# Performance work log

Hardware: AMD Instinct MI355X
Metric: run time of the kernel (lower is better)

## Reference

```python
import jax, jax.numpy as jnp
import numpy as np

# Planck radiance in wavenumber form: B(nu, T) = c1*nu^3 / (exp(c2*nu/T) - 1)
# nu in cm^-1, T in Kelvin, B in W / (m^2 sr cm^-1)
C1 = 1.191042e-8
C2 = 1.4387752
N_TEMPS = 20


def planck_radiance(nu, T):
    return C1 * nu ** 3 / jnp.expm1(C2 * nu / T)


def setup_inputs() -> dict:
    key = jax.random.key(0)
    k1, k2, k3 = jax.random.split(key, 3)
    N, C = 1048576, 54  # 1024x1024 pixels, 54 spectral channels
    wg = jnp.linspace(720.0, 1250.0, C, dtype=jnp.float32)
    v = (wg - wg.min()) / (wg.max() - wg.min())
    pi = 3.14159
    library = jnp.stack([
        jnp.full((C,), 0.98),                      # skin
        0.9 + 0.05 * jnp.sin(2 * pi * v),          # fabric_cotton
        0.15 + 0.1 * v,                            # metal_aluminum
        0.95 - 0.03 * v,                           # vegetation
        0.92 + 0.02 * jnp.sin(4 * pi * v),         # concrete
        0.85 + 0.1 * v,                            # glass
    ]).astype(jnp.float32)
    # realistic LWIR radiance magnitudes (~0.02-0.12 W/m^2/sr/cm^-1)
    s_sky = 0.05 * jax.random.uniform(k1, (C,), dtype=jnp.float32)
    s_ground = 0.08 + 0.02 * jax.random.uniform(k2, (C,), dtype=jnp.float32)
    s_obs = 0.02 + 0.1 * jax.random.uniform(k3, (N, C), dtype=jnp.float32)
    return {"s_obs": s_obs, "s_sky": s_sky, "s_ground": s_ground,
            "library": library, "wavenumber_grid": wg}


def reference(s_obs, s_sky, s_ground, library, wavenumber_grid):
    N, C = s_obs.shape
    M = library.shape[0]
    t_cand = jnp.linspace(250.0, 350.0, N_TEMPS, dtype=s_obs.dtype)
    # All candidate model spectra are pixel-independent (V fixed at 0.5):
    x_amb = 0.5 * s_sky + 0.5 * s_ground                           # [C]
    B = planck_radiance(wavenumber_grid[None, :], t_cand[:, None])  # [T, C]
    s_model = library[:, None, :] * B[None, :, :] \
        + (1.0 - library[:, None, :]) * x_amb                       # [M, T, C]
    cand = s_model.reshape(M * N_TEMPS, C)  # row-major: idx = m*T + t, matches loop order
    # ||s_obs - cand||^2 expanded: memory-bound [N, M*T] loss matrix
    losses = (jnp.sum(s_obs ** 2, axis=-1, keepdims=True)
              - 2.0 * s_obs @ cand.T
              + jnp.sum(cand ** 2, axis=-1))                        # [N, M*T]
    best = jnp.argmin(losses, axis=-1)                              # first-min, matches strict '<'
    best_loss = jnp.take_along_axis(losses, best[:, None], axis=1)[:, 0]
    m_idx = best // N_TEMPS
    t_idx = best % N_TEMPS
    best_t = t_cand[t_idx]                                          # [N]
    best_e = library[m_idx]                                         # [N, C]
    best_v = jnp.full((N,), 0.5, dtype=s_obs.dtype)
    s_recon = best_e * planck_radiance(wavenumber_grid[None, :], best_t[:, None]) \
        + (1.0 - best_e) * x_amb                                    # [N, C]
    texture = best_e.mean(axis=-1)
    beta = jnp.zeros((N, 1), dtype=s_obs.dtype)
    objective = best_loss.mean()
    return (best_t, best_e, best_v, beta, texture, s_recon, objective)
```

## Files before the change

kernel.cpp:

```cpp
#include <hip/hip_runtime.h>
#include <math.h>

#define C_CH 54
#define CP   64
#define NT   20
#define NM   6
#define NK   120
#define BLK  256

typedef float sf16 __attribute__((ext_vector_type(16)));
typedef float sf8  __attribute__((ext_vector_type(8)));

__global__ __launch_bounds__(256) void hadar_prep(
    const float* __restrict__ s_sky, const float* __restrict__ s_ground,
    const float* __restrict__ library, const float* __restrict__ wg,
    float* __restrict__ cand)
{
    __shared__ float xamb[C_CH];
    __shared__ float tc[NT];
    __shared__ float lm[NM];
    const int tid = threadIdx.x;
    if (tid < NT) tc[tid] = 250.0f + (float)tid * (100.0f / 19.0f);
    if (tid < C_CH) xamb[tid] = 0.5f * s_sky[tid] + 0.5f * s_ground[tid];
    if (tid < NM) {
        float s = 0.0f;
        for (int c = 0; c < C_CH; ++c) s += library[tid * C_CH + c];
        lm[tid] = s / (float)C_CH;
    }
    __syncthreads();

    const float c1 = 1.191042e-8f, c2 = 1.4387752f;
    for (int idx = tid; idx < NK * CP; idx += 256) {
        const int k = idx >> 6, c = idx & 63;
        float v = 0.0f;
        if (c < C_CH) {
            const int m = k / NT, t = k - m * NT;
            const float nu = wg[c];
            const float B = c1 * nu * nu * nu / expm1f(c2 * nu / tc[t]);
            const float e = library[m * C_CH + c];
            v = e * B + (1.0f - e) * xamb[c];
        }
        cand[idx] = v;
    }
    __syncthreads();

    if (tid < NK) {
        float s = 0.0f;
        for (int c = 0; c < C_CH; ++c) { float v = cand[tid * CP + c]; s += v * v; }
        const int m = tid / NT, t = tid - m * NT;
        cand[tid * CP + 54] = s;
        cand[tid * CP + 55] = tc[t];
        cand[tid * CP + 56] = lm[m];
    }
}

#define CE(c) ((c) < 16 ? q0[(c)] : (c) < 32 ? q1[(c)-16] : (c) < 48 ? q2[(c)-32] : q3[(c)-48])

__global__ __launch_bounds__(BLK) void hadar_main(
    const float* __restrict__ s_obs,
    const float* __restrict__ library,
    const float* __restrict__ cand,
    float* __restrict__ out, float* __restrict__ partials, int N)
{
    const int tid = threadIdx.x;
    const long long n0 = (long long)blockIdx.x * BLK + tid;
    const bool v0 = (n0 < N);

    float row0[C_CH];
    if (v0) {
        const float2* rp = (const float2*)(s_obs + n0 * C_CH);
        #pragma unroll
        for (int i = 0; i < C_CH / 2; ++i) {
            float2 w = rp[i];
            row0[2 * i] = w.x; row0[2 * i + 1] = w.y;
        }
    } else {
        #pragma unroll
        for (int c = 0; c < C_CH; ++c) row0[c] = 0.0f;
    }

    float ssq0 = 0.0f;
    #pragma unroll
    for (int c = 0; c < C_CH; ++c) ssq0 += row0[c] * row0[c];

    float bl0 = 3.4e38f;
    int bk0 = 0;

    const float* pk = cand;
    #pragma unroll 1
    for (int k = 0; k < NK; ++k, pk += CP) {
        sf16 q0, q1, q2;
        sf8  q3;
        asm volatile("s_load_dwordx16 %0, %1, 0x0"  : "=s"(q0) : "s"(pk));
        asm volatile("s_load_dwordx16 %0, %1, 0x40" : "=s"(q1) : "s"(pk));
        asm volatile("s_load_dwordx16 %0, %1, 0x80" : "=s"(q2) : "s"(pk));
        asm volatile("s_load_dwordx8  %0, %1, 0xc0" : "=s"(q3) : "s"(pk));
        asm volatile("s_waitcnt lgkmcnt(0)" : "+s"(q0), "+s"(q1), "+s"(q2), "+s"(q3));

        float a0[4] = {0.f, 0.f, 0.f, 0.f};
        #pragma unroll
        for (int c = 0; c < C_CH; ++c) {
            a0[c & 3] += row0[c] * CE(c);
        }
        const float sq = q3[6];
        const float d0 = (a0[0] + a0[1]) + (a0[2] + a0[3]);
        const float l0 = (ssq0 - 2.0f * d0) + sq;
        if (l0 < bl0) { bl0 = l0; bk0 = k; }
    }

    const size_t NN = (size_t)N;
    const size_t NC = (size_t)C_CH * NN;
    float lsum = 0.0f;

    if (v0) {
        lsum = bl0;
        const int m = bk0 / NT;
        const float* crow = cand + (size_t)bk0 * CP;

        out[n0] = crow[55];
        out[NN + NC + n0] = 0.5f;
        out[2 * NN + NC + n0] = 0.0f;
        out[3 * NN + NC + n0] = crow[56];

        float2* bep = (float2*)(out + NN + (size_t)n0 * C_CH);
        const float2* lp = (const float2*)(library + m * C_CH);
        #pragma unroll
        for (int i = 0; i < C_CH / 2; ++i) bep[i] = lp[i];

        float2* srp = (float2*)(out + 4 * NN + NC + (size_t)n0 * C_CH);
        const float2* cp2 = (const float2*)crow;
        #pragma unroll
        for (int i = 0; i < C_CH / 2; ++i) srp[i] = cp2[i];
    }

    __shared__ float red[BLK];
    red[tid] = lsum;
    __syncthreads();
    #pragma unroll
    for (int s = BLK / 2; s > 0; s >>= 1) {
        if (tid < s) red[tid] += red[tid + s];
        __syncthreads();
    }
    if (tid == 0) partials[blockIdx.x] = red[0];
}

__global__ __launch_bounds__(256) void hadar_reduce(
    const float* __restrict__ partials, int nb, float* __restrict__ obj_out, float invN)
{
    __shared__ float red[256];
    float s = 0.0f;
    for (int i = threadIdx.x; i < nb; i += 256) s += partials[i];
    red[threadIdx.x] = s;
    __syncthreads();
    #pragma unroll
    for (int st = 128; st > 0; st >>= 1) {
        if (threadIdx.x < st) red[threadIdx.x] += red[threadIdx.x + st];
        __syncthreads();
    }
    if (threadIdx.x == 0) *obj_out = red[0] * invN;
}

extern "C" void kernel_launch(void* const* d_in, const int* in_sizes, int n_in,
                              void* d_out, int out_size, void* d_ws, size_t ws_size,
                              hipStream_t stream)
{
    const float* s_obs    = (const float*)d_in[0];
    const float* s_sky    = (const float*)d_in[1];
    const float* s_ground = (const float*)d_in[2];
    const float* library  = (const float*)d_in[3];
    const float* wg       = (const float*)d_in[4];
    float* out = (float*)d_out;

    const int N  = in_sizes[0] / C_CH;
    const int nb = (N + BLK - 1) / BLK;

    float* ws       = (float*)d_ws;
    float* cand     = ws;
    float* partials = ws + 8192;

    hadar_prep<<<1, 256, 0, stream>>>(s_sky, s_ground, library, wg, cand);
    hadar_main<<<nb, BLK, 0, stream>>>(s_obs, library, cand, out, partials, N);

    const size_t NN = (size_t)N;
    float* obj_out = out + 4 * NN + 2 * (size_t)C_CH * NN;
    hadar_reduce<<<1, 256, 0, stream>>>(partials, nb, obj_out, 1.0f / (float)N);
}
```

Before: 852.1 us.

## Split each pixel across four lanes with DPP reductions and prescaled candidates

The main kernel now gives each pixel's 54-channel dot product to four lanes, each handling 16 channels. Partial sums are combined with DPP quad shuffles, and each lane processes two pixels so every candidate load is reused. Candidates are stored premultiplied by -2, with their squared norm folded in through a constant-1 input lane, which removes the per-candidate scale and add. Candidate data is read with vector loads instead of scalar loads, and writes are spread across lanes for better coalescing. The cost is 128 pixels per block instead of 256, a different rounding order, and redundant candidate loads across lanes.

Result: slower. 1.529 ms (+79.4%).

```diff
diff --git a/kernel.cpp b/kernel.cpp
--- a/kernel.cpp
+++ b/kernel.cpp
@@ -7,9 +7,17 @@
 #define NM   6
 #define NK   120
 #define BLK  256
-
-typedef float sf16 __attribute__((ext_vector_type(16)));
-typedef float sf8  __attribute__((ext_vector_type(8)));
+#define PIXW 32
+#define PPB  128
+
+__device__ __forceinline__ float qxor1(float v) {
+    return __int_as_float(__builtin_amdgcn_update_dpp(
+        __float_as_int(v), __float_as_int(v), 0xB1, 0xF, 0xF, true));
+}
+__device__ __forceinline__ float qxor2(float v) {
+    return __int_as_float(__builtin_amdgcn_update_dpp(
+        __float_as_int(v), __float_as_int(v), 0x4E, 0xF, 0xF, true));
+}
 
 __global__ __launch_bounds__(256) void hadar_prep(
     const float* __restrict__ s_sky, const float* __restrict__ s_ground,
@@ -32,29 +40,25 @@
     const float c1 = 1.191042e-8f, c2 = 1.4387752f;
     for (int idx = tid; idx < NK * CP; idx += 256) {
         const int k = idx >> 6, c = idx & 63;
+        const int m = k / NT, t = k - m * NT;
         float v = 0.0f;
         if (c < C_CH) {
-            const int m = k / NT, t = k - m * NT;
             const float nu = wg[c];
             const float B = c1 * nu * nu * nu / expm1f(c2 * nu / tc[t]);
             const float e = library[m * C_CH + c];
-            v = e * B + (1.0f - e) * xamb[c];
-        }
+            v = -2.0f * (e * B + (1.0f - e) * xamb[c]);
+        } else if (c == 56) v = tc[t];
+        else if (c == 57) v = lm[m];
         cand[idx] = v;
     }
     __syncthreads();
 
     if (tid < NK) {
         float s = 0.0f;
-        for (int c = 0; c < C_CH; ++c) { float v = cand[tid * CP + c]; s += v * v; }
-        const int m = tid / NT, t = tid - m * NT;
-        cand[tid * CP + 54] = s;
-        cand[tid * CP + 55] = tc[t];
-        cand[tid * CP + 56] = lm[m];
-    }
-}
-
-#define CE(c) ((c) < 16 ? q0[(c)] : (c) < 32 ? q1[(c)-16] : (c) < 48 ? q2[(c)-32] : q3[(c)-48])
+        for (int c = 0; c < C_CH; ++c) { float w = cand[tid * CP + c]; s += w * w; }
+        cand[tid * CP + 54] = 0.25f * s;
+    }
+}
 
 __global__ __launch_bounds__(BLK) void hadar_main(
     const float* __restrict__ s_obs,
@@ -62,75 +66,112 @@
     const float* __restrict__ cand,
     float* __restrict__ out, float* __restrict__ partials, int N)
 {
-    const int tid = threadIdx.x;
-    const long long n0 = (long long)blockIdx.x * BLK + tid;
-    const bool v0 = (n0 < N);
-
-    float row0[C_CH];
-    if (v0) {
-        const float2* rp = (const float2*)(s_obs + n0 * C_CH);
-        #pragma unroll
-        for (int i = 0; i < C_CH / 2; ++i) {
-            float2 w = rp[i];
-            row0[2 * i] = w.x; row0[2 * i + 1] = w.y;
-        }
-    } else {
-        #pragma unroll
-        for (int c = 0; c < C_CH; ++c) row0[c] = 0.0f;
-    }
-
-    float ssq0 = 0.0f;
-    #pragma unroll
-    for (int c = 0; c < C_CH; ++c) ssq0 += row0[c] * row0[c];
-
-    float bl0 = 3.4e38f;
-    int bk0 = 0;
-
-    const float* pk = cand;
-    #pragma unroll 1
-    for (int k = 0; k < NK; ++k, pk += CP) {
-        sf16 q0, q1, q2;
-        sf8  q3;
-        asm volatile("s_load_dwordx16 %0, %1, 0x0"  : "=s"(q0) : "s"(pk));
-        asm volatile("s_load_dwordx16 %0, %1, 0x40" : "=s"(q1) : "s"(pk));
-        asm volatile("s_load_dwordx16 %0, %1, 0x80" : "=s"(q2) : "s"(pk));
-        asm volatile("s_load_dwordx8  %0, %1, 0xc0" : "=s"(q3) : "s"(pk));
-        asm volatile("s_waitcnt lgkmcnt(0)" : "+s"(q0), "+s"(q1), "+s"(q2), "+s"(q3));
-
+    const int tid  = threadIdx.x;
+    const int wave = tid >> 6;
+    const int lane = tid & 63;
+    const int px   = lane >> 2;
+    const int g    = lane & 3;
+    const long long nb = (long long)blockIdx.x * PPB + wave * PIXW + px;
+
+    float r[2][16];
+    float ssq[2];
+    #pragma unroll
+    for (int p = 0; p < 2; ++p) {
+        const long long n = nb + p * 16;
+        #pragma unroll
+        for (int j = 0; j < 16; ++j) r[p][j] = 0.0f;
+        if (n < N) {
+            const float* src = s_obs + n * C_CH + g * 16;
+            if (g < 3) {
+                #pragma unroll
+                for (int j = 0; j < 8; ++j) {
+                    float2 w = *(const float2*)(src + 2 * j);
+                    r[p][2 * j] = w.x; r[p][2 * j + 1] = w.y;
+                }
+            } else {
+                #pragma unroll
+                for (int j = 0; j < 3; ++j) {
+                    float2 w = *(const float2*)(src + 2 * j);
+                    r[p][2 * j] = w.x; r[p][2 * j + 1] = w.y;
+                }
+            }
+        }
+        float s = 0.0f;
+        #pragma unroll
+        for (int j = 0; j < 16; ++j) s = fmaf(r[p][j], r[p][j], s);
+        s += qxor1(s);
+        s += qxor2(s);
+        ssq[p] = s;
+        if (g == 3) r[p][6] = 1.0f;
+    }
+
+    float bl[2] = { 3.4e38f, 3.4e38f };
+    int   bk[2] = { 0, 0 };
+
+    const float* cbase = cand + g * 16;
+    #pragma unroll 2
+    for (int k = 0; k < NK; ++k) {
+        const float* cp = cbase + (size_t)k * CP;
+        float cc[16];
+        #pragma unroll
+        for (int j = 0; j < 4; ++j) {
+            float4 w = *(const float4*)(cp + 4 * j);
+            cc[4 * j] = w.x; cc[4 * j + 1] = w.y; cc[4 * j + 2] = w.z; cc[4 * j + 3] = w.w;
+        }
         float a0[4] = {0.f, 0.f, 0.f, 0.f};
-        #pragma unroll
-        for (int c = 0; c < C_CH; ++c) {
-            a0[c & 3] += row0[c] * CE(c);
-        }
-        const float sq = q3[6];
-        const float d0 = (a0[0] + a0[1]) + (a0[2] + a0[3]);
-        const float l0 = (ssq0 - 2.0f * d0) + sq;
-        if (l0 < bl0) { bl0 = l0; bk0 = k; }
+        float a1[4] = {0.f, 0.f, 0.f, 0.f};
+        #pragma unroll
+        for (int j = 0; j < 16; ++j) {
+            a0[j & 3] = fmaf(r[0][j], cc[j], a0[j & 3]);
+            a1[j & 3] = fmaf(r[1][j], cc[j], a1[j & 3]);
+        }
+        float d0 = (a0[0] + a0[1]) + (a0[2] + a0[3]);
+        float d1 = (a1[0] + a1[1]) + (a1[2] + a1[3]);
+        d0 += qxor1(d0); d0 += qxor2(d0);
+        d1 += qxor1(d1); d1 += qxor2(d1);
+        if (d0 < bl[0]) { bl[0] = d0; bk[0] = k; }
+        if (d1 < bl[1]) { bl[1] = d1; bk[1] = k; }
     }
 
     const size_t NN = (size_t)N;
     const size_t NC = (size_t)C_CH * NN;
     float lsum = 0.0f;
-
-    if (v0) {
-        lsum = bl0;
-        const int m = bk0 / NT;
-        const float* crow = cand + (size_t)bk0 * CP;
-
-        out[n0] = crow[55];
-        out[NN + NC + n0] = 0.5f;
-        out[2 * NN + NC + n0] = 0.0f;
-        out[3 * NN + NC + n0] = crow[56];
-
-        float2* bep = (float2*)(out + NN + (size_t)n0 * C_CH);
-        const float2* lp = (const float2*)(library + m * C_CH);
-        #pragma unroll
-        for (int i = 0; i < C_CH / 2; ++i) bep[i] = lp[i];
-
-        float2* srp = (float2*)(out + 4 * NN + NC + (size_t)n0 * C_CH);
-        const float2* cp2 = (const float2*)crow;
-        #pragma unroll
-        for (int i = 0; i < C_CH / 2; ++i) srp[i] = cp2[i];
+    #pragma unroll
+    for (int p = 0; p < 2; ++p) {
+        const long long n = nb + p * 16;
+        if (n >= N) continue;
+        const int k = bk[p];
+        const int m = k / NT;
+        const float* crow = cand + (size_t)k * CP;
+
+        if (g == 0) {
+            out[n]                 = crow[56];
+            out[NN + NC + n]       = 0.5f;
+            out[2 * NN + NC + n]   = 0.0f;
+            out[3 * NN + NC + n]   = crow[57];
+            lsum += ssq[p] + bl[p];
+        }
+
+        const float* lrow = library + m * C_CH;
+        float* eout = out + NN + (size_t)n * C_CH;
+        float* rout = out + 4 * NN + NC + (size_t)n * C_CH;
+        if (g < 3) {
+            #pragma unroll
+            for (int j = 0; j < 8; ++j) {
+                const int c = g * 16 + 2 * j;
+                *(float2*)(eout + c) = *(const float2*)(lrow + c);
+                float2 w = *(const float2*)(crow + c);
+                *(float2*)(rout + c) = make_float2(-0.5f * w.x, -0.5f * w.y);
+            }
+        } else {
+            #pragma unroll
+            for (int j = 0; j < 3; ++j) {
+                const int c = 48 + 2 * j;
+                *(float2*)(eout + c) = *(const float2*)(lrow + c);
+                float2 w = *(const float2*)(crow + c);
+                *(float2*)(rout + c) = make_float2(-0.5f * w.x, -0.5f * w.y);
+            }
+        }
     }
 
     __shared__ float red[BLK];
@@ -172,7 +213,7 @@
     float* out = (float*)d_out;
 
     const int N  = in_sizes[0] / C_CH;
-    const int nb = (N + BLK - 1) / BLK;
+    const int nb = (N + PPB - 1) / PPB;
 
     float* ws       = (float*)d_ws;
     float* cand     = ws;
```
